# Performance work log

Measured on AMD Instinct MI355X. Metric: run time of the kernel, lower is better.

Reference implementation:

```python
import jax, jax.numpy as jnp
import numpy as np

EPS = 1e-7


def _make_boxes(key, b, n):
    k1, k2 = jax.random.split(key)
    xy = jax.random.uniform(k1, (b, n, 2), dtype=jnp.float32)
    wh = jax.random.uniform(k2, (b, n, 2), dtype=jnp.float32) * 0.2 + 0.01
    return jnp.concatenate([xy, xy + wh], axis=-1)  # [B,N,4] xyxy, valid boxes


def setup_inputs() -> dict:
    key = jax.random.key(0)
    kp, kt = jax.random.split(key)
    B, P, T = 64, 2048, 256
    return {
        "pred_bboxes": _make_boxes(kp, B, P),
        "target_bboxes": _make_boxes(kt, B, T),
    }


def _pairwise_cost(pred, target):
    # pred: [B,P,4], target: [B,T,4] -> cost [T,P] = mean_b (1 - IoU)
    p = pred[:, None, :, :]    # [B,1,P,4]
    t = target[:, :, None, :]  # [B,T,1,4]
    ix1 = jnp.maximum(p[..., 0], t[..., 0])
    iy1 = jnp.maximum(p[..., 1], t[..., 1])
    ix2 = jnp.minimum(p[..., 2], t[..., 2])
    iy2 = jnp.minimum(p[..., 3], t[..., 3])
    inter = jnp.clip(ix2 - ix1, 0.0) * jnp.clip(iy2 - iy1, 0.0)  # [B,T,P]
    area_p = (p[..., 2] - p[..., 0]) * (p[..., 3] - p[..., 1])
    area_t = (t[..., 2] - t[..., 0]) * (t[..., 3] - t[..., 1])
    union = area_p + area_t - inter
    iou = inter / (union + EPS)
    return jnp.mean(1.0 - iou, axis=0)  # [T,P]


def _greedy_match_loss(cost):
    # Sequential greedy: for each target (in order) pick the still-available
    # pred with minimal loss, remove it, accumulate. Matches the torch loop
    # (ties -> lowest index; 1-IoU losses are always >= 0).
    T, P = cost.shape

    def step(mask, cost_row):
        masked = jnp.where(mask, cost_row, jnp.inf)
        k = jnp.argmin(masked)
        loss = masked[k]
        return mask.at[k].set(False), loss

    _, losses = jax.lax.scan(step, jnp.ones((P,), dtype=bool), cost)
    return jnp.sum(losses) / T


def reference(pred_bboxes, target_bboxes):
    cost = _pairwise_cost(pred_bboxes, target_bboxes)  # [T,P]
    return _greedy_match_loss(cost)
```

## Files before the change

### kernel.cpp

```cpp
#include <hip/hip_runtime.h>
#include <hip/hip_bf16.h>

typedef unsigned long long u64;
typedef unsigned int u32;

#define NB 64
#define NP 2048
#define NT 256
#define TK 8
#define RB 8
#define TT 8
#define PB 128
#define EPSF 1e-7f

__device__ inline float iou1(const float4 pb, const float ap,
                             const float4 tb, const float at_eps) {
    float ix1 = fmaxf(pb.x, tb.x);
    float iy1 = fmaxf(pb.y, tb.y);
    float ix2 = fminf(pb.z, tb.z);
    float iy2 = fminf(pb.w, tb.w);
    float dx = fmaxf(ix2 - ix1, 0.f);
    float dy = fmaxf(iy2 - iy1, 0.f);
    float inter = dx * dy;
    float uni = (ap + at_eps) - inter;
    return inter * __builtin_amdgcn_rcpf(uni);
}

__global__ __launch_bounds__(512, 4) void cost_kernel(const float4* __restrict__ pred,
                                                      const float* __restrict__ tgt,
                                                      float* __restrict__ cost) {
    __shared__ float4 sT[NB * TT];
    __shared__ float sRed[8][TT][PB];
    const int tid = threadIdx.x;
    const int wv = tid >> 6, lane = tid & 63;
    const int p0 = blockIdx.x * PB + lane;
    const int t0 = blockIdx.y * TT;

    {
        int b = tid >> 3, tt = tid & 7;
        sT[tid] = *(const float4*)&tgt[(b * NT + t0 + tt) * 4];
    }
    __syncthreads();

    float acc0[TT] = {0.f, 0.f, 0.f, 0.f, 0.f, 0.f, 0.f, 0.f};
    float acc1[TT] = {0.f, 0.f, 0.f, 0.f, 0.f, 0.f, 0.f, 0.f};

    const int b0 = wv * 8;
#pragma unroll
    for (int i = 0; i < 8; ++i) {
        const int b = b0 + i;
        const float4 pa = pred[b * NP + p0];
        const float4 pc = pred[b * NP + p0 + 64];
        const float apa = (pa.z - pa.x) * (pa.w - pa.y);
        const float apc = (pc.z - pc.x) * (pc.w - pc.y);
#pragma unroll
        for (int tt = 0; tt < TT; ++tt) {
            const float4 tb = sT[b * TT + tt];
            const float at = (tb.z - tb.x) * (tb.w - tb.y) + EPSF;
            acc0[tt] += iou1(pa, apa, tb, at);
            acc1[tt] += iou1(pc, apc, tb, at);
        }
    }
#pragma unroll
    for (int tt = 0; tt < TT; ++tt) {
        sRed[wv][tt][lane] = acc0[tt];
        sRed[wv][tt][lane + 64] = acc1[tt];
    }
    __syncthreads();

    if (tid < 256) {
        const int tt = tid >> 5, q = tid & 31;
        float4 s = {0.f, 0.f, 0.f, 0.f};
#pragma unroll
        for (int w = 0; w < 8; ++w) {
            float4 a = *(const float4*)&sRed[w][tt][q * 4];
            s.x += a.x; s.y += a.y; s.z += a.z; s.w += a.w;
        }
        float4 c;
        c.x = 1.f - s.x * (1.f / NB);
        c.y = 1.f - s.y * (1.f / NB);
        c.z = 1.f - s.z * (1.f / NB);
        c.w = 1.f - s.w * (1.f / NB);
        *(float4*)&cost[(size_t)(t0 + tt) * NP + blockIdx.x * PB + q * 4] = c;
    }
}

__device__ inline u64 wave_min_u64(u64 k) {
#pragma unroll
    for (int off = 1; off < 64; off <<= 1) {
        u32 lo = (u32)__shfl_xor((int)(u32)k, off);
        u32 hi = (u32)__shfl_xor((int)(u32)(k >> 32), off);
        u64 o = ((u64)hi << 32) | lo;
        if (o < k) k = o;
    }
    return k;
}

__global__ __launch_bounds__(256) void topk_kernel(const float* __restrict__ cost,
                                                   u64* __restrict__ toplist) {
    __shared__ u64 sK[32];
    const int tid = threadIdx.x;
    const int wv = tid >> 6, lane = tid & 63;
    const int t = blockIdx.x;
    const float* row = cost + (size_t)t * NP;

    float v[8];
#pragma unroll
    for (int c = 0; c < 2; ++c) {
        float4 q = *(const float4*)(row + wv * 512 + c * 256 + 4 * lane);
        v[4 * c + 0] = q.x; v[4 * c + 1] = q.y;
        v[4 * c + 2] = q.z; v[4 * c + 3] = q.w;
    }
    u32 used = 0;
    for (int e = 0; e < TK; ++e) {
        u64 best = ~0ull;
        u32 bs = 0;
#pragma unroll
        for (int s = 0; s < 8; ++s) {
            u32 hb = ((used >> s) & 1u) ? 0xFFFFFFFFu : __float_as_uint(v[s]);
            u32 gidx = (u32)(wv * 512 + (s >> 2) * 256 + 4 * lane + (s & 3));
            u64 key = ((u64)hb << 32) | gidx;
            if (key < best) { best = key; bs = (u32)s; }
        }
        u64 g = wave_min_u64(best);
        if (best == g) used |= (1u << bs);
        if (lane == 0) sK[wv * TK + e] = g;
    }
    __syncthreads();
    if (wv == 0) {
        u64 k = (lane < 32) ? sK[lane] : ~0ull;
        for (int e = 0; e < TK; ++e) {
            u64 g = wave_min_u64(k);
            if (k == g) k = ~0ull;
            if (lane == 0) toplist[t * TK + e] = g;
        }
    }
}

__device__ __attribute__((noinline))
void fallback_pick(const float* __restrict__ row, u32 m, int lane,
                   u32* pickIdx, float* pickVal) {
    u64 best = ~0ull;
#pragma unroll 1
    for (int k = 0; k < 8; ++k) {
        float4 q = *(const float4*)(row + k * 256 + 4 * lane);
        float vv[4] = {q.x, q.y, q.z, q.w};
#pragma unroll
        for (int e = 0; e < 4; ++e) {
            u32 gidx = (u32)(k * 256 + 4 * lane + e);
            int w = __builtin_amdgcn_ds_bpermute((int)((gidx >> 5) << 2), (int)m);
            bool taken = (((u32)w >> (gidx & 31)) & 1u) != 0u;
            u32 hb = taken ? 0xFFFFFFFFu : __float_as_uint(vv[e]);
            u64 key = ((u64)hb << 32) | gidx;
            if (key < best) best = key;
        }
    }
    best = wave_min_u64(best);
    *pickIdx = (u32)best & (NP - 1);
    *pickVal = __uint_as_float((u32)(best >> 32));
}

__global__ __launch_bounds__(64) void greedy_kernel(const u64* __restrict__ toplist,
                                                    const float* __restrict__ cost,
                                                    float* __restrict__ out) {
    const int lane = threadIdx.x;

    u64 cur = toplist[lane];
    u32 m = 0;
    float sum = 0.f;
    u64 A = ~0ull;

#pragma unroll 1
    for (int k = 0; k < 32; ++k) {
        const u32 idx = (u32)cur & (NP - 1);
        const u32 vb = (u32)(cur >> 32);

        u64 nk = 0;
        int wn = 0;
        u32 idn = 0;
        if (k < 31) {
            nk = toplist[64 * (k + 1) + lane];
            idn = (u32)nk & (NP - 1);
            wn = __builtin_amdgcn_ds_bpermute((int)((idn >> 5) << 2), (int)m);
        }

        u32 pidx[RB]; float pval[RB];

        bool empty = false;
        int f[RB];
#pragma unroll
        for (int g = 0; g < RB; ++g) {
            u64 bal = A & (0xFFull << (8 * g));
            empty = empty || (bal == 0);
            f[g] = (int)__ffsll(bal) - 1;
        }
        bool ok = !empty;
        if (ok) {
#pragma unroll
            for (int g = 0; g < RB; ++g) {
                pidx[g] = (u32)__builtin_amdgcn_readlane((int)idx, f[g]);
                pval[g] = __uint_as_float((u32)__builtin_amdgcn_readlane((int)vb, f[g]));
            }
            u32 confl = 0;
#pragma unroll
            for (int g = 1; g < RB; ++g)
#pragma unroll
                for (int h = 0; h < g; ++h)
                    confl |= (pidx[g] == pidx[h]) ? 1u : 0u;
            ok = (confl == 0);
        }

        if (ok) {
#pragma unroll
            for (int g = 0; g < RB; ++g) {
                sum += pval[g];
                if ((pidx[g] >> 5) == (u32)lane) m |= (1u << (pidx[g] & 31));
            }
            if (k < 31) {
                bool availn = (((u32)wn >> (idn & 31)) & 1u) == 0u;
                bool hit = false;
#pragma unroll
                for (int g = 0; g < RB; ++g)
                    hit = hit || (idn == pidx[g]);
                A = __ballot(availn && !hit);
            }
        } else {
            u64 As = A;
#pragma unroll 1
            for (int gg = 0; gg < RB; ++gg) {
                u64 bal = As & (0xFFull << (8 * gg));
                u32 pi; float pv;
                if (bal != 0) {
                    int fs = (int)__ffsll(bal) - 1;
                    pi = (u32)__builtin_amdgcn_readlane((int)idx, fs);
                    pv = __uint_as_float((u32)__builtin_amdgcn_readlane((int)vb, fs));
                } else {
                    fallback_pick(cost + (size_t)(k * RB + gg) * NP, m, lane,
                                  &pi, &pv);
                }
                pidx[gg] = pi;
                pval[gg] = pv;
                sum += pv;
                if ((pi >> 5) == (u32)lane) m |= (1u << (pi & 31));
                As &= ~__ballot(idx == pi);
            }
            if (k < 31) {
                u64 An = __ballot((((u32)wn >> (idn & 31)) & 1u) == 0u);
#pragma unroll
                for (int g = 0; g < RB; ++g)
                    An &= ~__ballot(idn == pidx[g]);
                A = An;
            }
        }
        cur = nk;
    }
    if (lane == 0) out[0] = sum * (1.f / NT);
}

extern "C" void kernel_launch(void* const* d_in, const int* in_sizes, int n_in,
                              void* d_out, int out_size, void* d_ws, size_t ws_size,
                              hipStream_t stream) {
    const float4* pred = (const float4*)d_in[0];
    const float* tgt = (const float*)d_in[1];
    char* ws = (char*)d_ws;
    float* cost  = (float*)ws;
    u64* toplist = (u64*)(ws + (size_t)NT * NP * 4);

    cost_kernel<<<dim3(NP / PB, NT / TT), 512, 0, stream>>>(pred, tgt, cost);
    topk_kernel<<<NT, 256, 0, stream>>>(cost, toplist);
    greedy_kernel<<<1, 64, 0, stream>>>(toplist, cost, (float*)d_out);
}
```

Baseline: 55.86 us.

## Fuse cost computation with per-row top-k into one row kernel

Merges the cost and top-k kernels into a single kernel where each block computes one full target row (2048 preds, 1024 threads x 2) and immediately selects its top-8 from registers. This removes one kernel launch and the re-read of the cost matrix. The greedy kernel now preloads the whole toplist into registers and fully unrolls its loops. The trade-off is that pred data is now reread per target row with no reuse across targets in a block, and cost-stage parallelism drops from 512 blocks to 256.

```diff
diff --git a/kernel.cpp b/kernel.cpp
--- a/kernel.cpp
+++ b/kernel.cpp
@@ -9,8 +9,6 @@
 #define NT 256
 #define TK 8
 #define RB 8
-#define TT 8
-#define PB 128
 #define EPSF 1e-7f
 
 __device__ inline float iou1(const float4 pb, const float ap,
@@ -26,65 +24,6 @@
     return inter * __builtin_amdgcn_rcpf(uni);
 }
 
-__global__ __launch_bounds__(512, 4) void cost_kernel(const float4* __restrict__ pred,
-                                                      const float* __restrict__ tgt,
-                                                      float* __restrict__ cost) {
-    __shared__ float4 sT[NB * TT];
-    __shared__ float sRed[8][TT][PB];
-    const int tid = threadIdx.x;
-    const int wv = tid >> 6, lane = tid & 63;
-    const int p0 = blockIdx.x * PB + lane;
-    const int t0 = blockIdx.y * TT;
-
-    {
-        int b = tid >> 3, tt = tid & 7;
-        sT[tid] = *(const float4*)&tgt[(b * NT + t0 + tt) * 4];
-    }
-    __syncthreads();
-
-    float acc0[TT] = {0.f, 0.f, 0.f, 0.f, 0.f, 0.f, 0.f, 0.f};
-    float acc1[TT] = {0.f, 0.f, 0.f, 0.f, 0.f, 0.f, 0.f, 0.f};
-
-    const int b0 = wv * 8;
-#pragma unroll
-    for (int i = 0; i < 8; ++i) {
-        const int b = b0 + i;
-        const float4 pa = pred[b * NP + p0];
-        const float4 pc = pred[b * NP + p0 + 64];
-        const float apa = (pa.z - pa.x) * (pa.w - pa.y);
-        const float apc = (pc.z - pc.x) * (pc.w - pc.y);
-#pragma unroll
-        for (int tt = 0; tt < TT; ++tt) {
-            const float4 tb = sT[b * TT + tt];
-            const float at = (tb.z - tb.x) * (tb.w - tb.y) + EPSF;
-            acc0[tt] += iou1(pa, apa, tb, at);
-            acc1[tt] += iou1(pc, apc, tb, at);
-        }
-    }
-#pragma unroll
-    for (int tt = 0; tt < TT; ++tt) {
-        sRed[wv][tt][lane] = acc0[tt];
-        sRed[wv][tt][lane + 64] = acc1[tt];
-    }
-    __syncthreads();
-
-    if (tid < 256) {
-        const int tt = tid >> 5, q = tid & 31;
-        float4 s = {0.f, 0.f, 0.f, 0.f};
-#pragma unroll
-        for (int w = 0; w < 8; ++w) {
-            float4 a = *(const float4*)&sRed[w][tt][q * 4];
-            s.x += a.x; s.y += a.y; s.z += a.z; s.w += a.w;
-        }
-        float4 c;
-        c.x = 1.f - s.x * (1.f / NB);
-        c.y = 1.f - s.y * (1.f / NB);
-        c.z = 1.f - s.z * (1.f / NB);
-        c.w = 1.f - s.w * (1.f / NB);
-        *(float4*)&cost[(size_t)(t0 + tt) * NP + blockIdx.x * PB + q * 4] = c;
-    }
-}
-
 __device__ inline u64 wave_min_u64(u64 k) {
 #pragma unroll
     for (int off = 1; off < 64; off <<= 1) {
@@ -96,42 +35,67 @@
     return k;
 }
 
-__global__ __launch_bounds__(256) void topk_kernel(const float* __restrict__ cost,
+__global__ __launch_bounds__(1024) void row_kernel(const float4* __restrict__ pred,
+                                                   const float* __restrict__ tgt,
+                                                   float* __restrict__ cost,
                                                    u64* __restrict__ toplist) {
-    __shared__ u64 sK[32];
+    __shared__ float4 sT4[NB];
+    __shared__ float sA[NB];
+    __shared__ u64 sK[16 * TK];
     const int tid = threadIdx.x;
     const int wv = tid >> 6, lane = tid & 63;
     const int t = blockIdx.x;
-    const float* row = cost + (size_t)t * NP;
-
-    float v[8];
-#pragma unroll
-    for (int c = 0; c < 2; ++c) {
-        float4 q = *(const float4*)(row + wv * 512 + c * 256 + 4 * lane);
-        v[4 * c + 0] = q.x; v[4 * c + 1] = q.y;
-        v[4 * c + 2] = q.z; v[4 * c + 3] = q.w;
-    }
+
+    if (tid < NB) {
+        float4 tb = *(const float4*)&tgt[(tid * NT + t) * 4];
+        sT4[tid] = tb;
+        sA[tid] = (tb.z - tb.x) * (tb.w - tb.y) + EPSF;
+    }
+    __syncthreads();
+
+    float acc0 = 0.f, acc1 = 0.f;
+    for (int b = 0; b < NB; b += 4) {
+        float4 ps[8];
+#pragma unroll
+        for (int u = 0; u < 4; ++u) {
+            ps[2 * u]     = pred[(b + u) * NP + 2 * tid];
+            ps[2 * u + 1] = pred[(b + u) * NP + 2 * tid + 1];
+        }
+#pragma unroll
+        for (int u = 0; u < 4; ++u) {
+            const float4 tb = sT4[b + u];
+            const float at = sA[b + u];
+            acc0 += iou1(ps[2 * u], (ps[2 * u].z - ps[2 * u].x) * (ps[2 * u].w - ps[2 * u].y), tb, at);
+            acc1 += iou1(ps[2 * u + 1], (ps[2 * u + 1].z - ps[2 * u + 1].x) * (ps[2 * u + 1].w - ps[2 * u + 1].y), tb, at);
+        }
+    }
+    const float c0 = 1.f - acc0 * (1.f / NB);
+    const float c1 = 1.f - acc1 * (1.f / NB);
+    *(float2*)&cost[(size_t)t * NP + 2 * tid] = make_float2(c0, c1);
+
+    const u64 kA = ((u64)__float_as_uint(c0) << 32) | (u32)(2 * tid);
+    const u64 kB = ((u64)__float_as_uint(c1) << 32) | (u32)(2 * tid + 1);
     u32 used = 0;
     for (int e = 0; e < TK; ++e) {
-        u64 best = ~0ull;
-        u32 bs = 0;
-#pragma unroll
-        for (int s = 0; s < 8; ++s) {
-            u32 hb = ((used >> s) & 1u) ? 0xFFFFFFFFu : __float_as_uint(v[s]);
-            u32 gidx = (u32)(wv * 512 + (s >> 2) * 256 + 4 * lane + (s & 3));
-            u64 key = ((u64)hb << 32) | gidx;
-            if (key < best) { best = key; bs = (u32)s; }
-        }
+        u64 a = (used & 1u) ? ~0ull : kA;
+        u64 b = (used & 2u) ? ~0ull : kB;
+        u64 best = a < b ? a : b;
+        u32 bs = a < b ? 1u : 2u;
         u64 g = wave_min_u64(best);
-        if (best == g) used |= (1u << bs);
+        if (best == g) used |= bs;
         if (lane == 0) sK[wv * TK + e] = g;
     }
     __syncthreads();
     if (wv == 0) {
-        u64 k = (lane < 32) ? sK[lane] : ~0ull;
+        u64 kM0 = sK[2 * lane], kM1 = sK[2 * lane + 1];
+        u32 used2 = 0;
         for (int e = 0; e < TK; ++e) {
-            u64 g = wave_min_u64(k);
-            if (k == g) k = ~0ull;
+            u64 a = (used2 & 1u) ? ~0ull : kM0;
+            u64 b = (used2 & 2u) ? ~0ull : kM1;
+            u64 best = a < b ? a : b;
+            u32 bs = a < b ? 1u : 2u;
+            u64 g = wave_min_u64(best);
+            if (best == g) used2 |= bs;
             if (lane == 0) toplist[t * TK + e] = g;
         }
     }
@@ -164,23 +128,26 @@
                                                     const float* __restrict__ cost,
                                                     float* __restrict__ out) {
     const int lane = threadIdx.x;
-
-    u64 cur = toplist[lane];
+    u32 idxr[32], vbr[32];
+#pragma unroll
+    for (int k = 0; k < 32; ++k) {
+        u64 v = toplist[64 * k + lane];
+        idxr[k] = (u32)v & (NP - 1);
+        vbr[k] = (u32)(v >> 32);
+    }
+
     u32 m = 0;
     float sum = 0.f;
     u64 A = ~0ull;
 
-#pragma unroll 1
+#pragma unroll
     for (int k = 0; k < 32; ++k) {
-        const u32 idx = (u32)cur & (NP - 1);
-        const u32 vb = (u32)(cur >> 32);
-
-        u64 nk = 0;
+        const u32 idx = idxr[k];
+        const u32 vb = vbr[k];
         int wn = 0;
         u32 idn = 0;
         if (k < 31) {
-            nk = toplist[64 * (k + 1) + lane];
-            idn = (u32)nk & (NP - 1);
+            idn = idxr[k + 1];
             wn = __builtin_amdgcn_ds_bpermute((int)((idn >> 5) << 2), (int)m);
         }
 
@@ -226,7 +193,7 @@
             }
         } else {
             u64 As = A;
-#pragma unroll 1
+#pragma unroll
             for (int gg = 0; gg < RB; ++gg) {
                 u64 bal = As & (0xFFull << (8 * gg));
                 u32 pi; float pv;
@@ -252,7 +219,6 @@
                 A = An;
             }
         }
-        cur = nk;
     }
     if (lane == 0) out[0] = sum * (1.f / NT);
 }
@@ -266,7 +232,6 @@
     float* cost  = (float*)ws;
     u64* toplist = (u64*)(ws + (size_t)NT * NP * 4);
 
-    cost_kernel<<<dim3(NP / PB, NT / TT), 512, 0, stream>>>(pred, tgt, cost);
-    topk_kernel<<<NT, 256, 0, stream>>>(cost, toplist);
+    row_kernel<<<NT, 1024, 0, stream>>>(pred, tgt, cost, toplist);
     greedy_kernel<<<1, 64, 0, stream>>>(toplist, cost, (float*)d_out);
 }
```

New measurement: 52.56 us. 1.06x faster.
